# Kernel tuning notes

Hardware: AMD Instinct MI355X
Metric: run time of the kernel (lower is better)

## Reference

```python
import jax, jax.numpy as jnp
import numpy as np
from math import sqrt

B, TS_D, SEG, D, H = 16, 2, 1024, 256, 8
D_FF = 1024
DK = D // H
EPS = 1e-5


def _layernorm(x, g, b):
    mu = jnp.mean(x, axis=-1, keepdims=True)
    var = jnp.mean(jnp.square(x - mu), axis=-1, keepdims=True)
    return (x - mu) * jax.lax.rsqrt(var + EPS) * g + b


def setup_inputs() -> dict:
    key = jax.random.key(0)
    ks = jax.random.split(key, 16)
    s = 0.02
    return {
        "x": jax.random.normal(ks[0], (B, TS_D, SEG, D), dtype=jnp.float32),
        "Wq": jax.random.normal(ks[1], (D, D), dtype=jnp.float32) * s,
        "bq": jnp.zeros((D,), jnp.float32),
        "Wk": jax.random.normal(ks[2], (D, D), dtype=jnp.float32) * s,
        "bk": jnp.zeros((D,), jnp.float32),
        "Wv": jax.random.normal(ks[3], (D, D), dtype=jnp.float32) * s,
        "bv": jnp.zeros((D,), jnp.float32),
        "Wo": jax.random.normal(ks[4], (D, D), dtype=jnp.float32) * s,
        "bo": jnp.zeros((D,), jnp.float32),
        "g31": jnp.ones((D,), jnp.float32),
        "b31": jnp.zeros((D,), jnp.float32),
        "W1": jax.random.normal(ks[5], (D, D_FF), dtype=jnp.float32) * s,
        "b1": jnp.zeros((D_FF,), jnp.float32),
        "W2": jax.random.normal(ks[6], (D_FF, D), dtype=jnp.float32) * s,
        "b2": jnp.zeros((D,), jnp.float32),
        "g41": jnp.ones((D,), jnp.float32),
        "b41": jnp.zeros((D,), jnp.float32),
    }


def reference(x, Wq, bq, Wk, bk, Wv, bv, Wo, bo, g31, b31, W1, b1, W2, b2, g41, b41):
    # x: [B, ts_d=2, seg, d]; output is final_out2 (only live path of the module)
    b, ts_d, seg, d = x.shape
    scale = 1.0 / sqrt(DK)
    segments = x.reshape(b, ts_d * seg, d)            # [B, 2*seg, d]
    Q = (segments @ Wq + bq).reshape(b, -1, H, DK)
    K = (segments @ Wk + bk).reshape(b, -1, H, DK)
    V = (segments @ Wv + bv).reshape(b, -1, H, DK)
    q = Q[:, :seg]       # first seg positions (channel 0)
    k = K[:, -seg:]      # last seg positions (channel 1)
    v = V[:, -seg:]
    # cross-segment dual attention
    A1 = jax.nn.softmax(scale * jnp.einsum('blhe,bshe->bhls', q, k), axis=-1)
    out1 = jnp.einsum('bhls,bshd->blhd', A1, v).reshape(b, seg, d)
    A2 = jax.nn.softmax(scale * jnp.einsum('blhe,bshe->bhls', k, q), axis=-1)
    out2 = jnp.einsum('bhls,bshd->blhd', A2, q).reshape(b, seg, d)
    y = jnp.concatenate([out1, out2], axis=1) @ Wo + bo   # [B, 2*seg, d]
    h = _layernorm(segments + y, g31, b31)
    mlp = jax.nn.gelu(h @ W1 + b1, approximate=False) @ W2 + b2
    h = _layernorm(h + mlp, g41, b41)
    return h.reshape(b, ts_d, seg, d)
```

## Files before the change

### kernel.cpp

```cpp
#include <hip/hip_runtime.h>
#include <hip/hip_bf16.h>
#include <math.h>

#define BATCH 16
#define SEG 1024
#define DMODEL 256
#define NH 8
#define DK 32
#define DFF 1024
#define NTOK (BATCH * 2 * SEG)
#define EPS 1e-5f

typedef __attribute__((ext_vector_type(8))) short short8;
typedef __attribute__((ext_vector_type(4))) short short4b;
typedef __attribute__((ext_vector_type(4))) float f32x4;

#if __has_builtin(__builtin_amdgcn_exp2f)
#define EXP2(x) __builtin_amdgcn_exp2f(x)
#else
#define EXP2(x) __expf((x) * 0.6931471805599453f)
#endif

__device__ __forceinline__ ushort f2bf(float x) {
    union { float f; unsigned u; } a; a.f = x;
    unsigned r = a.u + 0x7fffu + ((a.u >> 16) & 1u);
    return (ushort)(r >> 16);
}

typedef const __attribute__((address_space(1))) unsigned gas_u32;
typedef __attribute__((address_space(3))) unsigned las_u32;
__device__ __forceinline__ void gload_lds16(const ushort* g, ushort* l) {
    __builtin_amdgcn_global_load_lds((gas_u32*)g, (las_u32*)l, 16, 0, 0);
}

__global__ __launch_bounds__(256) void wfrag_kernel(
    const float* __restrict__ src, ushort* __restrict__ dst, int K, int N, int order)
{
    const int tid = blockIdx.x * 256 + threadIdx.x;
    const int KT_ = K >> 5, NT_ = N >> 4;
    const int total = KT_ * NT_ * 64;
    if (tid >= total) return;
    const int lane = tid & 63;
    const int frag = tid >> 6;
    int kt, nt;
    if (order) { kt = frag / NT_; nt = frag % NT_; }
    else       { nt = frag / KT_; kt = frag % KT_; }
    const int quad = lane >> 4, l = lane & 15;
    const float* s = src + (size_t)(kt * 32 + quad * 8) * N + nt * 16 + l;
    short8 v;
#pragma unroll
    for (int j = 0; j < 8; j++) v[j] = (short)f2bf(s[(size_t)j * N]);
    *(short8*)&dst[(size_t)tid * 8] = v;
}

#define ASTR 264

__device__ __forceinline__ void dense256_pass(
    const ushort* __restrict__ Wf, ushort* WL, const short8* af,
    f32x4* acc, int t, int w, int lane)
{
#pragma unroll
    for (int nt = 0; nt < 16; ++nt) acc[nt] = (f32x4){0.f, 0.f, 0.f, 0.f};
    {
        const ushort* g = Wf + (size_t)w * 4096 + lane * 8;
        ushort* ld = WL + w * 4096;
#pragma unroll
        for (int i = 0; i < 8; ++i) gload_lds16(g + i * 512, ld + i * 512);
    }
    __syncthreads();
    for (int c = 0; c < 4; ++c) {
        if (c < 3) {
            const ushort* g = Wf + (size_t)(c + 1) * 16384 + w * 4096 + lane * 8;
            ushort* ld = WL + ((c + 1) & 1) * 8192 + w * 4096;
#pragma unroll
            for (int i = 0; i < 8; ++i) gload_lds16(g + i * 512, ld + i * 512);
        }
        const ushort* buf = WL + (c & 1) * 8192;
#pragma unroll
        for (int n2 = 0; n2 < 4; ++n2)
#pragma unroll
            for (int kt = 0; kt < 8; ++kt) {
                const short8 bf_ = *(const short8*)&buf[(n2 * 8 + kt) * 512 + lane * 8];
                acc[c * 4 + n2] = __builtin_amdgcn_mfma_f32_16x16x32_bf16(af[kt], bf_, acc[c * 4 + n2], 0, 0, 0);
            }
        __syncthreads();
    }
}

__global__ __launch_bounds__(256) void qkv_mfma_kernel(
    const float* __restrict__ x,
    const ushort* __restrict__ Wqf, const float* __restrict__ bq,
    const ushort* __restrict__ Wkf, const float* __restrict__ bk,
    const ushort* __restrict__ Wvf, const float* __restrict__ bv,
    ushort* __restrict__ qbuf, ushort* __restrict__ kbuf,
    ushort* __restrict__ qt, ushort* __restrict__ vt)
{
    __shared__ __align__(16) ushort SM[64 * ASTR];
    const int bid = blockIdx.x;
    const int which = bid >> 8;
    const int sub = bid & 255;
    const int b = sub >> 4, ti = sub & 15;
    const int half = (which == 0) ? 0 : 1;
    const int t = threadIdx.x;
    const int w = t >> 6, lane = t & 63, l = lane & 15, quad = lane >> 4;

    const float* xrow = x + ((size_t)b * 2048 + (size_t)half * 1024 + ti * 64) * 256;
#pragma unroll
    for (int p = 0; p < 16; ++p) {
        int ch = t + 256 * p;
        int row = ch >> 6, c4 = ch & 63;
        float4 v = *(const float4*)&xrow[row * 256 + c4 * 4];
        uint2 pk;
        pk.x = (unsigned)f2bf(v.x) | ((unsigned)f2bf(v.y) << 16);
        pk.y = (unsigned)f2bf(v.z) | ((unsigned)f2bf(v.w) << 16);
        *(uint2*)&SM[row * ASTR + c4 * 4] = pk;
    }
    __syncthreads();

    short8 af[8];
#pragma unroll
    for (int kt = 0; kt < 8; ++kt)
        af[kt] = *(const short8*)&SM[(w * 16 + l) * ASTR + kt * 32 + quad * 8];
    __syncthreads();

    const ushort* Wf  = (which == 0) ? Wqf : (which == 1 ? Wkf : Wvf);
    const float* bias = (which == 0) ? bq  : (which == 1 ? bk  : bv);
    const float kscale = (which == 1) ? 0.25503472f : 1.0f;

    f32x4 acc[16];
    dense256_pass(Wf, SM, af, acc, t, w, lane);

    ushort bfv[16][4];
#pragma unroll
    for (int nt = 0; nt < 16; ++nt) {
        const float bb = bias[nt * 16 + l];
#pragma unroll
        for (int r = 0; r < 4; ++r) bfv[nt][r] = f2bf((acc[nt][r] + bb) * kscale);
    }

    if (which <= 1) {
        ushort* obuf = which ? kbuf : qbuf;
#pragma unroll
        for (int nt = 0; nt < 16; ++nt) {
            const int h = nt >> 1, e = (nt & 1) * 16 + l;
#pragma unroll
            for (int r = 0; r < 4; ++r) {
                int tok = ti * 64 + w * 16 + quad * 4 + r;
                obuf[(((size_t)b * 8 + h) * SEG + tok) * 32 + e] = bfv[nt][r];
            }
        }
    }
    if (which != 1) {
        ushort* tb = which ? vt : qt;
#pragma unroll
        for (int nt = 0; nt < 16; ++nt)
#pragma unroll
            for (int r = 0; r < 4; ++r)
                SM[(nt * 16 + l) * 66 + w * 16 + quad * 4 + r] = bfv[nt][r];
        __syncthreads();
        const int d = t, hh = t >> 5, e = t & 31;
        ushort* dr = tb + (((size_t)b * 8 + hh) * 32 + e) * 1024 + ti * 64;
#pragma unroll
        for (int j = 0; j < 8; ++j) {
            uint2 v;
            v.x = *(const unsigned*)&SM[d * 66 + j * 8];
            v.y = *(const unsigned*)&SM[d * 66 + j * 8 + 2];
            unsigned z0 = *(const unsigned*)&SM[d * 66 + j * 8 + 4];
            unsigned z1 = *(const unsigned*)&SM[d * 66 + j * 8 + 6];
            *(uint4*)&dr[j * 8] = make_uint4(v.x, v.y, z0, z1);
        }
    }
}

#define KTILE 128
#define KP 40
#define VP 132

__global__ __launch_bounds__(256) void attn_mfma_kernel(
    const ushort* __restrict__ qbuf, const ushort* __restrict__ kbuf,
    const ushort* __restrict__ qt, const ushort* __restrict__ vt,
    ushort* __restrict__ abuf)
{
    __shared__ __align__(16) ushort Kl[KTILE * KP];
    __shared__ __align__(16) ushort Vl[32 * VP];

    const int bid   = blockIdx.x;
    const int sbh   = bid & 255;
    const int qtile = bid >> 8;
    const int stage = sbh >> 7;
    const int b     = (sbh >> 3) & 15;
    const int h     = sbh & 7;

    const ushort* Qm = stage ? kbuf : qbuf;
    const ushort* Km = stage ? qbuf : kbuf;
    const ushort* Vt = stage ? qt : vt;
    const size_t bh = ((size_t)b * 8 + h) * SEG * 32;

    const int t    = threadIdx.x;
    const int w    = t >> 6;
    const int lane = t & 63;
    const int l    = lane & 15;
    const int quad = lane >> 4;

    const int qrow = qtile * 64 + w * 16 + l;
    const short8 qf = *(const short8*)&Qm[bh + (size_t)qrow * 32 + quad * 8];

    f32x4 o0 = {0.f, 0.f, 0.f, 0.f};
    f32x4 o1 = {0.f, 0.f, 0.f, 0.f};
    f32x4 o2 = {0.f, 0.f, 0.f, 0.f};
    const short4b ones = {(short)0x3F80, (short)0x3F80, (short)0x3F80, (short)0x3F80};

    for (int tile = 0; tile < 8; ++tile) {
        __syncthreads();
        const ushort* Kg = &Km[bh + (size_t)(tile * KTILE) * 32];
#pragma unroll
        for (int p = 0; p < 2; ++p) {
            int ch = t + 256 * p;
            int row = ch >> 2, part = ch & 3;
            *(short8*)&Kl[row * KP + part * 8] = *(const short8*)&Kg[row * 32 + part * 8];
        }
        const ushort* Vg = &Vt[bh + (size_t)tile * KTILE];
#pragma unroll
        for (int p = 0; p < 2; ++p) {
            int ch = t + 256 * p;
            int d = ch >> 4, c = ch & 15;
            *(short8*)&Vl[d * VP + c * 8] = *(const short8*)&Vg[(size_t)d * 1024 + c * 8];
        }
        __syncthreads();

#pragma unroll
        for (int kb = 0; kb < 8; ++kb) {
            const short8 kf = *(const short8*)&Kl[(kb * 16 + l) * KP + quad * 8];
            f32x4 z = {0.f, 0.f, 0.f, 0.f};
            f32x4 sc = __builtin_amdgcn_mfma_f32_16x16x32_bf16(kf, qf, z, 0, 0, 0);
            union { float f; unsigned u; } a0, a1, a2, a3;
            a0.f = EXP2(sc[0]); a1.f = EXP2(sc[1]);
            a2.f = EXP2(sc[2]); a3.f = EXP2(sc[3]);
            unsigned lo = __builtin_amdgcn_perm(a1.u, a0.u, 0x07060302u);
            unsigned hi = __builtin_amdgcn_perm(a3.u, a2.u, 0x07060302u);
            union { uint2 u; short4b s; } pk; pk.u = make_uint2(lo, hi);
            const short4b vf0 = *(const short4b*)&Vl[l * VP + kb * 16 + quad * 4];
            const short4b vf1 = *(const short4b*)&Vl[(16 + l) * VP + kb * 16 + quad * 4];
            o0 = __builtin_amdgcn_mfma_f32_16x16x16bf16_1k(vf0, pk.s, o0, 0, 0, 0);
            o1 = __builtin_amdgcn_mfma_f32_16x16x16bf16_1k(vf1, pk.s, o1, 0, 0, 0);
            o2 = __builtin_amdgcn_mfma_f32_16x16x16bf16_1k(ones, pk.s, o2, 0, 0, 0);
        }
    }

    const float inv = 1.0f / o2[0];
#pragma unroll
    for (int r = 0; r < 4; ++r) { o0[r] *= inv; o1[r] *= inv; }

    __syncthreads();
    ushort* Ob = &Kl[w * 16 * 40];
#pragma unroll
    for (int r = 0; r < 4; ++r) {
        Ob[l * 40 + quad * 4 + r]      = f2bf(o0[r]);
        Ob[l * 40 + 16 + quad * 4 + r] = f2bf(o1[r]);
    }
    __syncthreads();
    const int q = lane >> 2, part = lane & 3;
    const short8 ov = *(const short8*)&Ob[q * 40 + part * 8];
    const int tok = qtile * 64 + w * 16 + q;
    *(short8*)&abuf[((size_t)b * 2 * SEG + (size_t)stage * SEG + tok) * 256 + h * 32 + part * 8] = ov;
}

__global__ __launch_bounds__(256) void proj_mfma_kernel(
    const ushort* __restrict__ abuf, const ushort* __restrict__ Wof,
    const float* __restrict__ bo, const float* __restrict__ x,
    const float* __restrict__ g31, const float* __restrict__ b31,
    float* __restrict__ hout)
{
    __shared__ __align__(16) ushort SM[64 * ASTR];
    const int bid = blockIdx.x;
    const size_t tok0 = (size_t)bid * 64;
    const int t = threadIdx.x;
    const int w = t >> 6, lane = t & 63, l = lane & 15, quad = lane >> 4;

#pragma unroll
    for (int p = 0; p < 8; ++p) {
        int ch = t + 256 * p;
        int row = ch >> 5, c8 = ch & 31;
        *(short8*)&SM[row * ASTR + c8 * 8] = *(const short8*)&abuf[(tok0 + row) * 256 + c8 * 8];
    }
    __syncthreads();

    short8 af[8];
#pragma unroll
    for (int kt = 0; kt < 8; ++kt)
        af[kt] = *(const short8*)&SM[(w * 16 + l) * ASTR + kt * 32 + quad * 8];
    __syncthreads();

    f32x4 acc[16];
    dense256_pass(Wof, SM, af, acc, t, w, lane);

#pragma unroll
    for (int nt = 0; nt < 16; ++nt) {
        const int d = nt * 16 + l;
        const float bv = bo[d];
#pragma unroll
        for (int r = 0; r < 4; ++r) {
            size_t tok = tok0 + w * 16 + quad * 4 + r;
            acc[nt][r] += bv + x[tok * 256 + d];
        }
    }

    float mu_[4], is_[4];
#pragma unroll
    for (int r = 0; r < 4; ++r) {
        float s = 0.f;
#pragma unroll
        for (int nt = 0; nt < 16; ++nt) s += acc[nt][r];
        s += __shfl_xor(s, 1); s += __shfl_xor(s, 2);
        s += __shfl_xor(s, 4); s += __shfl_xor(s, 8);
        float mu = s * (1.0f / 256.0f);
        float vs = 0.f;
#pragma unroll
        for (int nt = 0; nt < 16; ++nt) { float dd = acc[nt][r] - mu; vs += dd * dd; }
        vs += __shfl_xor(vs, 1); vs += __shfl_xor(vs, 2);
        vs += __shfl_xor(vs, 4); vs += __shfl_xor(vs, 8);
        mu_[r] = mu;
        is_[r] = rsqrtf(vs * (1.0f / 256.0f) + EPS);
    }

#pragma unroll
    for (int nt = 0; nt < 16; ++nt) {
        const int d = nt * 16 + l;
        const float gg = g31[d], bb = b31[d];
#pragma unroll
        for (int r = 0; r < 4; ++r) {
            size_t tok = tok0 + w * 16 + quad * 4 + r;
            hout[tok * 256 + d] = (acc[nt][r] - mu_[r]) * is_[r] * gg + bb;
        }
    }
}

#define GP 40

__global__ __launch_bounds__(256) void mlp_mfma_kernel(
    const float* __restrict__ W1dummy_unused, const ushort* __restrict__ W1f,
    const float* __restrict__ b1, const ushort* __restrict__ W2f,
    const float* __restrict__ b2, const float* __restrict__ g41,
    const float* __restrict__ b41, float* __restrict__ io)
{
    __shared__ __align__(16) ushort SM[2 * 16384];
    __shared__ __align__(16) ushort G[4][16 * GP];
    __shared__ __align__(16) float B1L[DFF];
    const int bid = blockIdx.x;
    const size_t tok0 = (size_t)bid * 64;
    const int t = threadIdx.x;
    const int w = t >> 6, lane = t & 63, l = lane & 15, quad = lane >> 4;

    const float* hrow = io + tok0 * 256;
#pragma unroll
    for (int p = 0; p < 16; ++p) {
        int ch = t + 256 * p;
        int row = ch >> 6, c4 = ch & 63;
        float4 v = *(const float4*)&hrow[row * 256 + c4 * 4];
        uint2 pk;
        pk.x = (unsigned)f2bf(v.x) | ((unsigned)f2bf(v.y) << 16);
        pk.y = (unsigned)f2bf(v.z) | ((unsigned)f2bf(v.w) << 16);
        *(uint2*)&SM[row * ASTR + c4 * 4] = pk;
    }
    *(float4*)&B1L[t * 4] = *(const float4*)&b1[t * 4];
    __syncthreads();

    short8 af[8];
#pragma unroll
    for (int kt = 0; kt < 8; ++kt)
        af[kt] = *(const short8*)&SM[(w * 16 + l) * ASTR + kt * 32 + quad * 8];
    __syncthreads();

    f32x4 out[16];
#pragma unroll
    for (int nt = 0; nt < 16; ++nt) out[nt] = (f32x4){0.f, 0.f, 0.f, 0.f};

    ushort* Gw = &G[w][0];

    {
        const ushort* g1 = W1f + w * 2048 + lane * 8;
        const ushort* g2 = W2f + w * 2048 + lane * 8;
        ushort* l1 = SM + w * 2048;
        ushort* l2 = SM + 8192 + w * 2048;
#pragma unroll
        for (int i = 0; i < 4; ++i) {
            gload_lds16(g1 + i * 512, l1 + i * 512);
            gload_lds16(g2 + i * 512, l2 + i * 512);
        }
    }
    __syncthreads();

    for (int c = 0; c < 32; ++c) {
        if (c < 31) {
            const int nb = (c + 1) & 1;
            const ushort* g1 = W1f + (size_t)(c + 1) * 8192 + w * 2048 + lane * 8;
            ushort* l1 = SM + nb * 16384 + w * 2048;
            const ushort* g2 = W2f + (size_t)(c + 1) * 8192 + w * 2048 + lane * 8;
            ushort* l2 = SM + nb * 16384 + 8192 + w * 2048;
#pragma unroll
            for (int i = 0; i < 4; ++i) {
                gload_lds16(g1 + i * 512, l1 + i * 512);
                gload_lds16(g2 + i * 512, l2 + i * 512);
            }
        }
        const ushort* WL = SM + (c & 1) * 16384;

        f32x4 s[2];
        s[0] = (f32x4){0.f, 0.f, 0.f, 0.f};
        s[1] = (f32x4){0.f, 0.f, 0.f, 0.f};
#pragma unroll
        for (int n2 = 0; n2 < 2; ++n2)
#pragma unroll
            for (int kt = 0; kt < 8; ++kt) {
                const short8 bf_ = *(const short8*)&WL[(n2 * 8 + kt) * 512 + lane * 8];
                s[n2] = __builtin_amdgcn_mfma_f32_16x16x32_bf16(af[kt], bf_, s[n2], 0, 0, 0);
            }

#pragma unroll
        for (int n2 = 0; n2 < 2; ++n2) {
            const float bv = B1L[c * 32 + n2 * 16 + l];
#pragma unroll
            for (int r = 0; r < 4; ++r) {
                float v = s[n2][r] + bv;
                float au = fabsf(v) * 0.70710678118654752f;
                float t1 = __builtin_amdgcn_rcpf(fmaf(0.3275911f, au, 1.0f));
                float e  = EXP2(au * au * -1.4426950408889634f);
                float p5 = fmaf(fmaf(fmaf(fmaf(1.061405429f, t1, -1.453152027f),
                                t1, 1.421413741f), t1, -0.284496736f), t1, 0.254829592f) * t1;
                float erf_abs = fmaf(-p5, e, 1.0f);
                float gl = fmaf(0.5f * fabsf(v), erf_abs, 0.5f * v);
                Gw[(quad * 4 + r) * GP + n2 * 16 + l] = f2bf(gl);
            }
        }

        const short8 gf = *(const short8*)&Gw[l * GP + quad * 8];
#pragma unroll
        for (int nt = 0; nt < 16; ++nt) {
            const short8 bf_ = *(const short8*)&WL[8192 + nt * 512 + lane * 8];
            out[nt] = __builtin_amdgcn_mfma_f32_16x16x32_bf16(gf, bf_, out[nt], 0, 0, 0);
        }
        __syncthreads();
    }

#pragma unroll
    for (int nt = 0; nt < 16; ++nt) {
        const int d = nt * 16 + l;
        const float bv = b2[d];
#pragma unroll
        for (int r = 0; r < 4; ++r) {
            size_t tok = tok0 + w * 16 + quad * 4 + r;
            out[nt][r] += bv + io[tok * 256 + d];
        }
    }

    float mu_[4], is_[4];
#pragma unroll
    for (int r = 0; r < 4; ++r) {
        float s = 0.f;
#pragma unroll
        for (int nt = 0; nt < 16; ++nt) s += out[nt][r];
        s += __shfl_xor(s, 1); s += __shfl_xor(s, 2);
        s += __shfl_xor(s, 4); s += __shfl_xor(s, 8);
        float mu = s * (1.0f / 256.0f);
        float vs = 0.f;
#pragma unroll
        for (int nt = 0; nt < 16; ++nt) { float dd = out[nt][r] - mu; vs += dd * dd; }
        vs += __shfl_xor(vs, 1); vs += __shfl_xor(vs, 2);
        vs += __shfl_xor(vs, 4); vs += __shfl_xor(vs, 8);
        mu_[r] = mu;
        is_[r] = rsqrtf(vs * (1.0f / 256.0f) + EPS);
    }

#pragma unroll
    for (int nt = 0; nt < 16; ++nt) {
        const int d = nt * 16 + l;
        const float gg = g41[d], bb = b41[d];
#pragma unroll
        for (int r = 0; r < 4; ++r) {
            size_t tok = tok0 + w * 16 + quad * 4 + r;
            io[tok * 256 + d] = (out[nt][r] - mu_[r]) * is_[r] * gg + bb;
        }
    }
}

extern "C" void kernel_launch(void* const* d_in, const int* in_sizes, int n_in,
                              void* d_out, int out_size, void* d_ws, size_t ws_size,
                              hipStream_t stream)
{
    const float* x   = (const float*)d_in[0];
    const float* Wq  = (const float*)d_in[1];
    const float* bq  = (const float*)d_in[2];
    const float* Wk  = (const float*)d_in[3];
    const float* bk  = (const float*)d_in[4];
    const float* Wv  = (const float*)d_in[5];
    const float* bv  = (const float*)d_in[6];
    const float* Wo  = (const float*)d_in[7];
    const float* bo  = (const float*)d_in[8];
    const float* g31 = (const float*)d_in[9];
    const float* b31 = (const float*)d_in[10];
    const float* W1  = (const float*)d_in[11];
    const float* b1  = (const float*)d_in[12];
    const float* W2  = (const float*)d_in[13];
    const float* b2  = (const float*)d_in[14];
    const float* g41 = (const float*)d_in[15];
    const float* b41 = (const float*)d_in[16];

    float* out = (float*)d_out;

    const size_t HALF = (size_t)BATCH * SEG * DMODEL;
    ushort* qbuf = (ushort*)d_ws;
    ushort* kbuf = qbuf + HALF;
    ushort* qt   = kbuf + HALF;
    ushort* vt   = qt + HALF;
    ushort* abuf = vt + HALF;
    ushort* Wqf  = abuf + 2 * HALF;
    ushort* Wkf  = Wqf + 65536;
    ushort* Wvf  = Wkf + 65536;
    ushort* Wof  = Wvf + 65536;
    ushort* W1f  = Wof + 65536;
    ushort* W2f  = W1f + 262144;

    wfrag_kernel<<<32, 256, 0, stream>>>(Wq, Wqf, 256, 256, 0);
    wfrag_kernel<<<32, 256, 0, stream>>>(Wk, Wkf, 256, 256, 0);
    wfrag_kernel<<<32, 256, 0, stream>>>(Wv, Wvf, 256, 256, 0);
    wfrag_kernel<<<32, 256, 0, stream>>>(Wo, Wof, 256, 256, 0);
    wfrag_kernel<<<128, 256, 0, stream>>>(W1, W1f, 256, 1024, 0);
    wfrag_kernel<<<128, 256, 0, stream>>>(W2, W2f, 1024, 256, 1);

    qkv_mfma_kernel<<<768, 256, 0, stream>>>(x, Wqf, bq, Wkf, bk, Wvf, bv,
                                             qbuf, kbuf, qt, vt);
    attn_mfma_kernel<<<2 * BATCH * NH * (SEG / 64), 256, 0, stream>>>(qbuf, kbuf, qt, vt, abuf);
    proj_mfma_kernel<<<NTOK / 64, 256, 0, stream>>>(abuf, Wof, bo, x, g31, b31, out);
    mlp_mfma_kernel<<<NTOK / 64, 256, 0, stream>>>(nullptr, W1f, b1, W2f, b2, g41, b41, out);
}
```

Baseline: 284.9 us.

## Split MLP kernel across 8 waves, halving per-wave hidden and output columns

The MLP kernel now launches 512 threads per block, with waves paired so each handles half of the hidden chunk columns and half of the output columns for the same 16 tokens. This halves per-wave accumulator registers and per-wave loads, which should raise occupancy and the number of waves available to hide latency. Cross-wave LayerNorm reduction now goes through shared memory using a single-pass sum and sum-of-squares variance. In exchange, each chunk needs an extra barrier, and the single-pass variance is less numerically robust.

```diff
diff --git a/kernel.cpp b/kernel.cpp
--- a/kernel.cpp
+++ b/kernel.cpp
@@ -337,7 +337,7 @@
 
 #define GP 40
 
-__global__ __launch_bounds__(256) void mlp_mfma_kernel(
+__global__ __launch_bounds__(512, 4) void mlp_mfma_kernel(
     const float* __restrict__ W1dummy_unused, const ushort* __restrict__ W1f,
     const float* __restrict__ b1, const ushort* __restrict__ W2f,
     const float* __restrict__ b2, const float* __restrict__ g41,
@@ -346,15 +346,17 @@
     __shared__ __align__(16) ushort SM[2 * 16384];
     __shared__ __align__(16) ushort G[4][16 * GP];
     __shared__ __align__(16) float B1L[DFF];
+    __shared__ float PS[2][2][4][16];
     const int bid = blockIdx.x;
     const size_t tok0 = (size_t)bid * 64;
     const int t = threadIdx.x;
     const int w = t >> 6, lane = t & 63, l = lane & 15, quad = lane >> 4;
+    const int wt = w & 3, wh = w >> 2;
 
     const float* hrow = io + tok0 * 256;
 #pragma unroll
-    for (int p = 0; p < 16; ++p) {
-        int ch = t + 256 * p;
+    for (int p = 0; p < 8; ++p) {
+        int ch = t + 512 * p;
         int row = ch >> 6, c4 = ch & 63;
         float4 v = *(const float4*)&hrow[row * 256 + c4 * 4];
         uint2 pk;
@@ -362,66 +364,55 @@
         pk.y = (unsigned)f2bf(v.z) | ((unsigned)f2bf(v.w) << 16);
         *(uint2*)&SM[row * ASTR + c4 * 4] = pk;
     }
-    *(float4*)&B1L[t * 4] = *(const float4*)&b1[t * 4];
+    *(float2*)&B1L[t * 2] = *(const float2*)&b1[t * 2];
     __syncthreads();
 
     short8 af[8];
 #pragma unroll
     for (int kt = 0; kt < 8; ++kt)
-        af[kt] = *(const short8*)&SM[(w * 16 + l) * ASTR + kt * 32 + quad * 8];
-    __syncthreads();
-
-    f32x4 out[16];
-#pragma unroll
-    for (int nt = 0; nt < 16; ++nt) out[nt] = (f32x4){0.f, 0.f, 0.f, 0.f};
-
-    ushort* Gw = &G[w][0];
+        af[kt] = *(const short8*)&SM[(wt * 16 + l) * ASTR + kt * 32 + quad * 8];
+    __syncthreads();
+
+    f32x4 out[8];
+#pragma unroll
+    for (int nt = 0; nt < 8; ++nt) out[nt] = (f32x4){0.f, 0.f, 0.f, 0.f};
+
+    ushort* Gw = &G[wt][0];
 
     {
-        const ushort* g1 = W1f + w * 2048 + lane * 8;
-        const ushort* g2 = W2f + w * 2048 + lane * 8;
-        ushort* l1 = SM + w * 2048;
-        ushort* l2 = SM + 8192 + w * 2048;
-#pragma unroll
-        for (int i = 0; i < 4; ++i) {
-            gload_lds16(g1 + i * 512, l1 + i * 512);
-            gload_lds16(g2 + i * 512, l2 + i * 512);
-        }
+        const ushort* g1 = W1f + w * 1024 + lane * 8;
+        const ushort* g2 = W2f + w * 1024 + lane * 8;
+        ushort* l1 = SM + w * 1024;
+        ushort* l2 = SM + 8192 + w * 1024;
+        gload_lds16(g1, l1); gload_lds16(g1 + 512, l1 + 512);
+        gload_lds16(g2, l2); gload_lds16(g2 + 512, l2 + 512);
     }
     __syncthreads();
 
     for (int c = 0; c < 32; ++c) {
         if (c < 31) {
             const int nb = (c + 1) & 1;
-            const ushort* g1 = W1f + (size_t)(c + 1) * 8192 + w * 2048 + lane * 8;
-            ushort* l1 = SM + nb * 16384 + w * 2048;
-            const ushort* g2 = W2f + (size_t)(c + 1) * 8192 + w * 2048 + lane * 8;
-            ushort* l2 = SM + nb * 16384 + 8192 + w * 2048;
-#pragma unroll
-            for (int i = 0; i < 4; ++i) {
-                gload_lds16(g1 + i * 512, l1 + i * 512);
-                gload_lds16(g2 + i * 512, l2 + i * 512);
-            }
+            const ushort* g1 = W1f + (size_t)(c + 1) * 8192 + w * 1024 + lane * 8;
+            ushort* l1 = SM + nb * 16384 + w * 1024;
+            const ushort* g2 = W2f + (size_t)(c + 1) * 8192 + w * 1024 + lane * 8;
+            ushort* l2 = SM + nb * 16384 + 8192 + w * 1024;
+            gload_lds16(g1, l1); gload_lds16(g1 + 512, l1 + 512);
+            gload_lds16(g2, l2); gload_lds16(g2 + 512, l2 + 512);
         }
         const ushort* WL = SM + (c & 1) * 16384;
 
-        f32x4 s[2];
-        s[0] = (f32x4){0.f, 0.f, 0.f, 0.f};
-        s[1] = (f32x4){0.f, 0.f, 0.f, 0.f};
-#pragma unroll
-        for (int n2 = 0; n2 < 2; ++n2)
-#pragma unroll
-            for (int kt = 0; kt < 8; ++kt) {
-                const short8 bf_ = *(const short8*)&WL[(n2 * 8 + kt) * 512 + lane * 8];
-                s[n2] = __builtin_amdgcn_mfma_f32_16x16x32_bf16(af[kt], bf_, s[n2], 0, 0, 0);
-            }
-
-#pragma unroll
-        for (int n2 = 0; n2 < 2; ++n2) {
-            const float bv = B1L[c * 32 + n2 * 16 + l];
+        f32x4 s = {0.f, 0.f, 0.f, 0.f};
+#pragma unroll
+        for (int kt = 0; kt < 8; ++kt) {
+            const short8 bf_ = *(const short8*)&WL[(wh * 8 + kt) * 512 + lane * 8];
+            s = __builtin_amdgcn_mfma_f32_16x16x32_bf16(af[kt], bf_, s, 0, 0, 0);
+        }
+
+        {
+            const float bv = B1L[c * 32 + wh * 16 + l];
 #pragma unroll
             for (int r = 0; r < 4; ++r) {
-                float v = s[n2][r] + bv;
+                float v = s[r] + bv;
                 float au = fabsf(v) * 0.70710678118654752f;
                 float t1 = __builtin_amdgcn_rcpf(fmaf(0.3275911f, au, 1.0f));
                 float e  = EXP2(au * au * -1.4426950408889634f);
@@ -429,55 +420,65 @@
                                 t1, 1.421413741f), t1, -0.284496736f), t1, 0.254829592f) * t1;
                 float erf_abs = fmaf(-p5, e, 1.0f);
                 float gl = fmaf(0.5f * fabsf(v), erf_abs, 0.5f * v);
-                Gw[(quad * 4 + r) * GP + n2 * 16 + l] = f2bf(gl);
+                Gw[(quad * 4 + r) * GP + wh * 16 + l] = f2bf(gl);
             }
         }
+        __syncthreads();
 
         const short8 gf = *(const short8*)&Gw[l * GP + quad * 8];
 #pragma unroll
-        for (int nt = 0; nt < 16; ++nt) {
-            const short8 bf_ = *(const short8*)&WL[8192 + nt * 512 + lane * 8];
+        for (int nt = 0; nt < 8; ++nt) {
+            const short8 bf_ = *(const short8*)&WL[8192 + (wh * 8 + nt) * 512 + lane * 8];
             out[nt] = __builtin_amdgcn_mfma_f32_16x16x32_bf16(gf, bf_, out[nt], 0, 0, 0);
         }
         __syncthreads();
     }
 
 #pragma unroll
-    for (int nt = 0; nt < 16; ++nt) {
-        const int d = nt * 16 + l;
+    for (int nt = 0; nt < 8; ++nt) {
+        const int d = (wh * 8 + nt) * 16 + l;
         const float bv = b2[d];
 #pragma unroll
         for (int r = 0; r < 4; ++r) {
-            size_t tok = tok0 + w * 16 + quad * 4 + r;
+            size_t tok = tok0 + wt * 16 + quad * 4 + r;
             out[nt][r] += bv + io[tok * 256 + d];
         }
     }
 
+#pragma unroll
+    for (int r = 0; r < 4; ++r) {
+        float s1 = 0.f, s2 = 0.f;
+#pragma unroll
+        for (int nt = 0; nt < 8; ++nt) { float v = out[nt][r]; s1 += v; s2 += v * v; }
+        s1 += __shfl_xor(s1, 1); s1 += __shfl_xor(s1, 2);
+        s1 += __shfl_xor(s1, 4); s1 += __shfl_xor(s1, 8);
+        s2 += __shfl_xor(s2, 1); s2 += __shfl_xor(s2, 2);
+        s2 += __shfl_xor(s2, 4); s2 += __shfl_xor(s2, 8);
+        if (l == 0) {
+            PS[0][wh][wt][quad * 4 + r] = s1;
+            PS[1][wh][wt][quad * 4 + r] = s2;
+        }
+    }
+    __syncthreads();
+
     float mu_[4], is_[4];
 #pragma unroll
     for (int r = 0; r < 4; ++r) {
-        float s = 0.f;
-#pragma unroll
-        for (int nt = 0; nt < 16; ++nt) s += out[nt][r];
-        s += __shfl_xor(s, 1); s += __shfl_xor(s, 2);
-        s += __shfl_xor(s, 4); s += __shfl_xor(s, 8);
-        float mu = s * (1.0f / 256.0f);
-        float vs = 0.f;
-#pragma unroll
-        for (int nt = 0; nt < 16; ++nt) { float dd = out[nt][r] - mu; vs += dd * dd; }
-        vs += __shfl_xor(vs, 1); vs += __shfl_xor(vs, 2);
-        vs += __shfl_xor(vs, 4); vs += __shfl_xor(vs, 8);
+        float s1 = PS[0][0][wt][quad * 4 + r] + PS[0][1][wt][quad * 4 + r];
+        float s2 = PS[1][0][wt][quad * 4 + r] + PS[1][1][wt][quad * 4 + r];
+        float mu = s1 * (1.0f / 256.0f);
+        float var = s2 * (1.0f / 256.0f) - mu * mu;
         mu_[r] = mu;
-        is_[r] = rsqrtf(vs * (1.0f / 256.0f) + EPS);
-    }
-
-#pragma unroll
-    for (int nt = 0; nt < 16; ++nt) {
-        const int d = nt * 16 + l;
+        is_[r] = rsqrtf(var + EPS);
+    }
+
+#pragma unroll
+    for (int nt = 0; nt < 8; ++nt) {
+        const int d = (wh * 8 + nt) * 16 + l;
         const float gg = g41[d], bb = b41[d];
 #pragma unroll
         for (int r = 0; r < 4; ++r) {
-            size_t tok = tok0 + w * 16 + quad * 4 + r;
+            size_t tok = tok0 + wt * 16 + quad * 4 + r;
             io[tok * 256 + d] = (out[nt][r] - mu_[r]) * is_[r] * gg + bb;
         }
     }
@@ -531,5 +532,5 @@
                                              qbuf, kbuf, qt, vt);
     attn_mfma_kernel<<<2 * BATCH * NH * (SEG / 64), 256, 0, stream>>>(qbuf, kbuf, qt, vt, abuf);
     proj_mfma_kernel<<<NTOK / 64, 256, 0, stream>>>(abuf, Wof, bo, x, g31, b31, out);
-    mlp_mfma_kernel<<<NTOK / 64, 256, 0, stream>>>(nullptr, W1f, b1, W2f, b2, g41, b41, out);
-}
+    mlp_mfma_kernel<<<NTOK / 64, 512, 0, stream>>>(nullptr, W1f, b1, W2f, b2, g41, b41, out);
+}
```

Result: faster. 274.7 us (-3.6%).

## Retile MLP kernel into 2x2 warp grid and reorder attention K tile loads

Applied to the files above, without the earlier changes.

The MLP kernel now arranges its four warps as a 2x2 grid: each warp handles 32 tokens and half of the FFN chunk or output columns. Each B-fragment read from LDS therefore feeds two MFMAs, and the per-warp accumulators shrink from 16 to 8 tiles per row-block. This adds a block-wide barrier per chunk to share the GELU tile, and the LayerNorm now combines partial sums through shared memory using a single-pass variance formula, which is slightly less numerically robust. Launch bounds request two blocks per CU, and the attention kernel's K tile load uses a different thread-to-row mapping, likely to change the global access or LDS bank pattern.

```diff
diff --git a/kernel.cpp b/kernel.cpp
--- a/kernel.cpp
+++ b/kernel.cpp
@@ -216,7 +216,8 @@
 #pragma unroll
         for (int p = 0; p < 2; ++p) {
             int ch = t + 256 * p;
-            int row = ch >> 2, part = ch & 3;
+            int row = ((ch >> 6) << 4) | (ch & 15);
+            int part = (ch >> 4) & 3;
             *(short8*)&Kl[row * KP + part * 8] = *(const short8*)&Kg[row * 32 + part * 8];
         }
         const ushort* Vg = &Vt[bh + (size_t)tile * KTILE];
@@ -337,19 +338,21 @@
 
 #define GP 40
 
-__global__ __launch_bounds__(256) void mlp_mfma_kernel(
+__global__ __launch_bounds__(256, 2) void mlp_mfma_kernel(
     const float* __restrict__ W1dummy_unused, const ushort* __restrict__ W1f,
     const float* __restrict__ b1, const ushort* __restrict__ W2f,
     const float* __restrict__ b2, const float* __restrict__ g41,
     const float* __restrict__ b41, float* __restrict__ io)
 {
     __shared__ __align__(16) ushort SM[2 * 16384];
-    __shared__ __align__(16) ushort G[4][16 * GP];
+    __shared__ __align__(16) ushort G[64 * GP];
     __shared__ __align__(16) float B1L[DFF];
+    __shared__ float PS[2][2][64];
     const int bid = blockIdx.x;
     const size_t tok0 = (size_t)bid * 64;
     const int t = threadIdx.x;
     const int w = t >> 6, lane = t & 63, l = lane & 15, quad = lane >> 4;
+    const int g = w >> 1, f = w & 1;
 
     const float* hrow = io + tok0 * 256;
 #pragma unroll
@@ -365,17 +368,19 @@
     *(float4*)&B1L[t * 4] = *(const float4*)&b1[t * 4];
     __syncthreads();
 
-    short8 af[8];
-#pragma unroll
-    for (int kt = 0; kt < 8; ++kt)
-        af[kt] = *(const short8*)&SM[(w * 16 + l) * ASTR + kt * 32 + quad * 8];
-    __syncthreads();
-
-    f32x4 out[16];
-#pragma unroll
-    for (int nt = 0; nt < 16; ++nt) out[nt] = (f32x4){0.f, 0.f, 0.f, 0.f};
-
-    ushort* Gw = &G[w][0];
+    short8 af[2][8];
+#pragma unroll
+    for (int j = 0; j < 2; ++j)
+#pragma unroll
+        for (int kt = 0; kt < 8; ++kt)
+            af[j][kt] = *(const short8*)&SM[(g * 32 + j * 16 + l) * ASTR + kt * 32 + quad * 8];
+    __syncthreads();
+
+    f32x4 out[2][8];
+#pragma unroll
+    for (int j = 0; j < 2; ++j)
+#pragma unroll
+        for (int nt = 0; nt < 8; ++nt) out[j][nt] = (f32x4){0.f, 0.f, 0.f, 0.f};
 
     {
         const ushort* g1 = W1f + w * 2048 + lane * 8;
@@ -405,23 +410,21 @@
         }
         const ushort* WL = SM + (c & 1) * 16384;
 
-        f32x4 s[2];
-        s[0] = (f32x4){0.f, 0.f, 0.f, 0.f};
-        s[1] = (f32x4){0.f, 0.f, 0.f, 0.f};
-#pragma unroll
-        for (int n2 = 0; n2 < 2; ++n2)
-#pragma unroll
-            for (int kt = 0; kt < 8; ++kt) {
-                const short8 bf_ = *(const short8*)&WL[(n2 * 8 + kt) * 512 + lane * 8];
-                s[n2] = __builtin_amdgcn_mfma_f32_16x16x32_bf16(af[kt], bf_, s[n2], 0, 0, 0);
-            }
-
-#pragma unroll
-        for (int n2 = 0; n2 < 2; ++n2) {
-            const float bv = B1L[c * 32 + n2 * 16 + l];
+        f32x4 s0 = {0.f, 0.f, 0.f, 0.f};
+        f32x4 s1 = {0.f, 0.f, 0.f, 0.f};
+#pragma unroll
+        for (int kt = 0; kt < 8; ++kt) {
+            const short8 bf_ = *(const short8*)&WL[(f * 8 + kt) * 512 + lane * 8];
+            s0 = __builtin_amdgcn_mfma_f32_16x16x32_bf16(af[0][kt], bf_, s0, 0, 0, 0);
+            s1 = __builtin_amdgcn_mfma_f32_16x16x32_bf16(af[1][kt], bf_, s1, 0, 0, 0);
+        }
+
+        const float bv = B1L[c * 32 + f * 16 + l];
+#pragma unroll
+        for (int j = 0; j < 2; ++j) {
 #pragma unroll
             for (int r = 0; r < 4; ++r) {
-                float v = s[n2][r] + bv;
+                float v = (j ? s1[r] : s0[r]) + bv;
                 float au = fabsf(v) * 0.70710678118654752f;
                 float t1 = __builtin_amdgcn_rcpf(fmaf(0.3275911f, au, 1.0f));
                 float e  = EXP2(au * au * -1.4426950408889634f);
@@ -429,58 +432,79 @@
                                 t1, 1.421413741f), t1, -0.284496736f), t1, 0.254829592f) * t1;
                 float erf_abs = fmaf(-p5, e, 1.0f);
                 float gl = fmaf(0.5f * fabsf(v), erf_abs, 0.5f * v);
-                Gw[(quad * 4 + r) * GP + n2 * 16 + l] = f2bf(gl);
-            }
-        }
-
-        const short8 gf = *(const short8*)&Gw[l * GP + quad * 8];
-#pragma unroll
-        for (int nt = 0; nt < 16; ++nt) {
-            const short8 bf_ = *(const short8*)&WL[8192 + nt * 512 + lane * 8];
-            out[nt] = __builtin_amdgcn_mfma_f32_16x16x32_bf16(gf, bf_, out[nt], 0, 0, 0);
+                G[(g * 32 + j * 16 + quad * 4 + r) * GP + f * 16 + l] = f2bf(gl);
+            }
         }
         __syncthreads();
-    }
-
-#pragma unroll
-    for (int nt = 0; nt < 16; ++nt) {
-        const int d = nt * 16 + l;
-        const float bv = b2[d];
+
+        const short8 gf0 = *(const short8*)&G[(g * 32 + l) * GP + quad * 8];
+        const short8 gf1 = *(const short8*)&G[(g * 32 + 16 + l) * GP + quad * 8];
+#pragma unroll
+        for (int nt = 0; nt < 8; ++nt) {
+            const short8 bf_ = *(const short8*)&WL[8192 + (f * 8 + nt) * 512 + lane * 8];
+            out[0][nt] = __builtin_amdgcn_mfma_f32_16x16x32_bf16(gf0, bf_, out[0][nt], 0, 0, 0);
+            out[1][nt] = __builtin_amdgcn_mfma_f32_16x16x32_bf16(gf1, bf_, out[1][nt], 0, 0, 0);
+        }
+        __syncthreads();
+    }
+
+#pragma unroll
+    for (int j = 0; j < 2; ++j)
+#pragma unroll
+        for (int nt = 0; nt < 8; ++nt) {
+            const int d = f * 128 + nt * 16 + l;
+            const float bvv = b2[d];
+#pragma unroll
+            for (int r = 0; r < 4; ++r) {
+                size_t tok = tok0 + g * 32 + j * 16 + quad * 4 + r;
+                out[j][nt][r] += bvv + io[tok * 256 + d];
+            }
+        }
+
+#pragma unroll
+    for (int j = 0; j < 2; ++j)
 #pragma unroll
         for (int r = 0; r < 4; ++r) {
-            size_t tok = tok0 + w * 16 + quad * 4 + r;
-            out[nt][r] += bv + io[tok * 256 + d];
-        }
-    }
-
-    float mu_[4], is_[4];
-#pragma unroll
-    for (int r = 0; r < 4; ++r) {
-        float s = 0.f;
-#pragma unroll
-        for (int nt = 0; nt < 16; ++nt) s += out[nt][r];
-        s += __shfl_xor(s, 1); s += __shfl_xor(s, 2);
-        s += __shfl_xor(s, 4); s += __shfl_xor(s, 8);
-        float mu = s * (1.0f / 256.0f);
-        float vs = 0.f;
-#pragma unroll
-        for (int nt = 0; nt < 16; ++nt) { float dd = out[nt][r] - mu; vs += dd * dd; }
-        vs += __shfl_xor(vs, 1); vs += __shfl_xor(vs, 2);
-        vs += __shfl_xor(vs, 4); vs += __shfl_xor(vs, 8);
-        mu_[r] = mu;
-        is_[r] = rsqrtf(vs * (1.0f / 256.0f) + EPS);
-    }
-
-#pragma unroll
-    for (int nt = 0; nt < 16; ++nt) {
-        const int d = nt * 16 + l;
-        const float gg = g41[d], bb = b41[d];
+            float p1 = 0.f, p2 = 0.f;
+#pragma unroll
+            for (int nt = 0; nt < 8; ++nt) { float v = out[j][nt][r]; p1 += v; p2 += v * v; }
+            p1 += __shfl_xor(p1, 1); p1 += __shfl_xor(p1, 2);
+            p1 += __shfl_xor(p1, 4); p1 += __shfl_xor(p1, 8);
+            p2 += __shfl_xor(p2, 1); p2 += __shfl_xor(p2, 2);
+            p2 += __shfl_xor(p2, 4); p2 += __shfl_xor(p2, 8);
+            if (l == 0) {
+                PS[0][f][g * 32 + j * 16 + quad * 4 + r] = p1;
+                PS[1][f][g * 32 + j * 16 + quad * 4 + r] = p2;
+            }
+        }
+    __syncthreads();
+
+    float mu_[2][4], is_[2][4];
+#pragma unroll
+    for (int j = 0; j < 2; ++j)
 #pragma unroll
         for (int r = 0; r < 4; ++r) {
-            size_t tok = tok0 + w * 16 + quad * 4 + r;
-            io[tok * 256 + d] = (out[nt][r] - mu_[r]) * is_[r] * gg + bb;
-        }
-    }
+            int tk = g * 32 + j * 16 + quad * 4 + r;
+            float S1 = PS[0][0][tk] + PS[0][1][tk];
+            float S2 = PS[1][0][tk] + PS[1][1][tk];
+            float mu = S1 * (1.0f / 256.0f);
+            float var = S2 * (1.0f / 256.0f) - mu * mu;
+            mu_[j][r] = mu;
+            is_[j][r] = rsqrtf(var + EPS);
+        }
+
+#pragma unroll
+    for (int j = 0; j < 2; ++j)
+#pragma unroll
+        for (int nt = 0; nt < 8; ++nt) {
+            const int d = f * 128 + nt * 16 + l;
+            const float gg = g41[d], bb = b41[d];
+#pragma unroll
+            for (int r = 0; r < 4; ++r) {
+                size_t tok = tok0 + g * 32 + j * 16 + quad * 4 + r;
+                io[tok * 256 + d] = (out[j][nt][r] - mu_[j][r]) * is_[j][r] * gg + bb;
+            }
+        }
 }
 
 extern "C" void kernel_launch(void* const* d_in, const int* in_sizes, int n_in,
```

After: 283.8 us. No clear change (-0.4%).
